# Kernel optimization log

Measured on AMD Instinct MI355X. Metric: run time of the kernel, lower is better.

The kernel has to match this reference:

```python
import jax, jax.numpy as jnp
import numpy as np

B, C, W, H, Z = 2, 32, 96, 96, 64
IC = C  # inter_channels defaults to in_channels (required by depthwise g conv)
THRESH = 1.5
EPS = 1e-5


def setup_inputs() -> dict:
    key = jax.random.key(0)
    ks = jax.random.split(key, 12)
    s1 = 1.0 / np.sqrt(C)   # 1x1x1 conv fan-in
    s3 = 1.0 / np.sqrt(3.0) # depthwise (1,1,3) conv fan-in per channel
    return {
        "x": jax.random.normal(ks[0], (B, C, W, H, Z), jnp.float32),
        # per-sample spacings in [0,3): mixes both branches around thresh 1.5
        "spacings": jax.random.uniform(ks[1], (B, 3), jnp.float32) * 3.0,
        "theta_w": jax.random.normal(ks[2], (IC, C), jnp.float32) * s1,
        "theta_b": jax.random.normal(ks[3], (IC,), jnp.float32) * s1,
        "phi_w": jax.random.normal(ks[4], (IC, C), jnp.float32) * s1,
        "phi_b": jax.random.normal(ks[5], (IC,), jnp.float32) * s1,
        "g_w": jax.random.normal(ks[6], (C, 3), jnp.float32) * s3,   # depthwise kernel along z
        "g_b": jax.random.normal(ks[7], (C,), jnp.float32) * s3,
        "W_w": jax.random.normal(ks[8], (C, IC), jnp.float32) * s1,
        "W_b": jax.random.normal(ks[9], (C,), jnp.float32) * s1,
        # torch inits BN gamma=0, beta=0 (zero-init residual trick); use small random
        "bn_gamma": jax.random.normal(ks[10], (C,), jnp.float32) * 0.1,
        "bn_beta": jax.random.normal(ks[11], (C,), jnp.float32) * 0.1,
    }


def _cvec(v):
    return v.reshape(1, -1, 1, 1, 1)


def _conv1x1(h, w, b):
    # 1x1x1 Conv3d == channel-mixing matmul
    return jnp.einsum('bcwhz,oc->bowhz', h, w) + _cvec(b)


def reference(x, spacings, theta_w, theta_b, phi_w, phi_b, g_w, g_b, W_w, W_b, bn_gamma, bn_beta):
    # theta/phi: 1x1x1 convs -> (B, IC, W, H, Z)
    t = _conv1x1(x, theta_w, theta_b)
    p = _conv1x1(x, phi_w, phi_b)

    # g: depthwise conv along z, kernel 3, pad 1 (groups=C)
    xp = jnp.pad(x, ((0, 0), (0, 0), (0, 0), (0, 0), (1, 1)))
    gx = (xp[..., :-2] * _cvec(g_w[:, 0])
          + xp[..., 1:-1] * _cvec(g_w[:, 1])
          + xp[..., 2:] * _cvec(g_w[:, 2])
          + _cvec(g_b))

    # non-local attention along z per (b, w, h) row: scores (B, W, H, Z, Z)
    f = jnp.einsum('bcwhz,bcwhy->bwhzy', t, p)
    a = jax.nn.softmax(f, axis=-1)
    y = jnp.einsum('bwhzy,bcwhy->bcwhz', a, gx)
    nl = y + x  # residual inside compute_x

    # per-sample branch on z-spacing, vectorized with where
    mask = (spacings[:, -1] <= THRESH).reshape(-1, 1, 1, 1, 1)
    res = jnp.where(mask, nl, x)

    # W: 1x1x1 conv + BatchNorm3d (training-mode batch stats)
    out = _conv1x1(res, W_w, W_b)
    mean = jnp.mean(out, axis=(0, 2, 3, 4), keepdims=True)
    var = jnp.var(out, axis=(0, 2, 3, 4), keepdims=True)
    out = (out - mean) * jax.lax.rsqrt(var + EPS)
    return out * _cvec(bn_gamma) + _cvec(bn_beta)
```

## Files before the change

kernel.cpp:

```cpp
#include <hip/hip_runtime.h>
#include <stdint.h>

#define CHS 589824
#define ROWS 18432
#define WHn 9216
#define NRED 1179648.0f
#define LOG2E 1.4426950408889634f

typedef short s16x8 __attribute__((ext_vector_type(8)));
typedef float f32x4v __attribute__((ext_vector_type(4)));

#define MFMA16 __builtin_amdgcn_mfma_f32_16x16x32_bf16

#define WSFRAG 10240

#define OXH 0
#define OP  8704
#define OG  13312
#define ROWL 17664
#define LDSZ (2*ROWL)

static __device__ __forceinline__ uint16_t bfh(float v) {
    union { __bf16 h; uint16_t u; } c; c.h = (__bf16)v; return c.u;
}
static __device__ __forceinline__ float bf2f(uint16_t u) {
    union { uint32_t x; float f; } c; c.x = (uint32_t)u << 16; return c.f;
}
static __device__ __forceinline__ uint32_t pk2u(uint16_t a, uint16_t b) {
    return (uint32_t)a | ((uint32_t)b << 16);
}
static __device__ __forceinline__ uint32_t pkbf(float a, float b) {
    return pk2u(bfh(a), bfh(b));
}
static __device__ __forceinline__ float ex2(float x) {
    float r;
    asm("v_exp_f32 %0, %1" : "=v"(r) : "v"(x));
    return r;
}
static __device__ __forceinline__ s16x8 rd8(const char* p) {
    union { uint64_t q[2]; s16x8 s; } v;
    v.q[0] = *(const uint64_t*)p;
    v.q[1] = *(const uint64_t*)(p + 8);
    return v.s;
}

static __device__ __forceinline__ void wfrag2(const float* __restrict__ Wp, int mt, int l15, int kb,
                                              float sc, s16x8& hi, s16x8& lo) {
    const float* p = Wp + (l15 + 16*mt)*32 + 8*kb;
    const float4 f0 = *(const float4*)p;
    const float4 f1 = *(const float4*)(p + 4);
    float f[8] = {f0.x*sc, f0.y*sc, f0.z*sc, f0.w*sc, f1.x*sc, f1.y*sc, f1.z*sc, f1.w*sc};
    union { uint32_t u[4]; s16x8 v; } rh, rl;
    #pragma unroll
    for (int i = 0; i < 4; ++i) {
        const uint16_t h0 = bfh(f[2*i]), h1 = bfh(f[2*i+1]);
        rh.u[i] = pk2u(h0, h1);
        rl.u[i] = pk2u(bfh(f[2*i] - bf2f(h0)), bfh(f[2*i+1] - bf2f(h1)));
    }
    hi = rh.v; lo = rl.v;
}
static __device__ __forceinline__ s16x8 wfragW(const float* __restrict__ Wp, int mt, int l15, int kb) {
    const float* p = Wp + (l15 + 16*mt)*32;
    const float4 f0 = *(const float4*)(p + 4*kb);
    const float4 f1 = *(const float4*)(p + 16 + 4*kb);
    union { uint32_t u[4]; s16x8 v; } r;
    r.u[0] = pkbf(f0.x, f0.y); r.u[1] = pkbf(f0.z, f0.w);
    r.u[2] = pkbf(f1.x, f1.y); r.u[3] = pkbf(f1.z, f1.w);
    return r.v;
}

__global__ __launch_bounds__(256) void k0_frag(
    const float* __restrict__ theta_w, const float* __restrict__ phi_w,
    const float* __restrict__ Ww, char* __restrict__ ws)
{
    const int tid = threadIdx.x;
    const int m = tid >> 7;
    const int r = tid & 127;
    const int mt = r >> 6, l = r & 63;
    s16x8 hi, lo;
    wfrag2(m ? phi_w : theta_w, mt, l & 15, l >> 4, m ? 1.0f : LOG2E, hi, lo);
    *(s16x8*)(ws + m*4096 + (mt*64 + l)*16)        = hi;
    *(s16x8*)(ws + m*4096 + 2048 + (mt*64 + l)*16) = lo;
    if (tid < 128) {
        const int mtw = tid >> 6, lw = tid & 63;
        *(s16x8*)(ws + 8192 + (mtw*64 + lw)*16) = wfragW(Ww, mtw, lw & 15, lw >> 4);
    }
}

__global__ __launch_bounds__(256, 4) void k1_row(
    const float* __restrict__ x, const float* __restrict__ spacings,
    const float* __restrict__ theta_b, const float* __restrict__ phi_b,
    const float* __restrict__ g_w, const float* __restrict__ g_b,
    const float* __restrict__ Wb, const char* __restrict__ frags,
    float* __restrict__ out, float* __restrict__ part)
{
    __shared__ __align__(16) char lds[LDSZ];
    const int t = threadIdx.x;
    const int wv = t >> 6, l = t & 63;
    const int l15 = l & 15, kb = l >> 4;
    const int row0 = blockIdx.x*2;
    const int b = row0 / WHn, wh = row0 - b*WHn;
    const long base = (long)b*32*CHS + (long)wh*64;
    const int zr = 16*wv + l15;

    #pragma unroll
    for (int rr = 0; rr < 2; ++rr) {
        char* L = lds + rr*ROWL;
        const float* xp = x + base + rr*64;
        float xv[8];
        #pragma unroll
        for (int j = 0; j < 8; ++j) xv[j] = xp[(long)(8*wv + j)*CHS + l];
        #pragma unroll
        for (int j = 0; j < 4; ++j) {
            const uint16_t h0 = bfh(xv[2*j]), h1 = bfh(xv[2*j+1]);
            *(uint32_t*)(L + OXH + l*136 + (8*wv + 2*j)*2)      = pk2u(h0, h1);
            *(uint32_t*)(L + OXH + l*136 + 64 + (8*wv + 2*j)*2) =
                pk2u(bfh(xv[2*j] - bf2f(h0)), bfh(xv[2*j+1] - bf2f(h1)));
        }
        const int pG = 32*(l >> 5) + 8*((l >> 2) & 3) + 4*((l >> 4) & 1) + (l & 3);
        #pragma unroll
        for (int j = 0; j < 8; ++j) {
            const int c = 8*wv + j;
            float xm = __shfl_up(xv[j], 1);   if (l == 0)  xm = 0.f;
            float xp2 = __shfl_down(xv[j], 1); if (l == 63) xp2 = 0.f;
            const float g = g_w[3*c]*xm + g_w[3*c+1]*xv[j] + g_w[3*c+2]*xp2 + g_b[c];
            *(uint16_t*)(L + OG + c*136 + 2*pG) = bfh(g);
        }
    }
    __syncthreads();

    s16x8 bth[2], btl[2];
    {
        s16x8 bxh[2], bxl[2];
        #pragma unroll
        for (int rr = 0; rr < 2; ++rr) {
            bxh[rr] = rd8(lds + rr*ROWL + OXH + zr*136 + 16*kb);
            bxl[rr] = rd8(lds + rr*ROWL + OXH + zr*136 + 64 + 16*kb);
        }
        {
            const s16x8 t0h = *(const s16x8*)(frags + l*16);
            const s16x8 t1h = *(const s16x8*)(frags + 1024 + l*16);
            const s16x8 t0l = *(const s16x8*)(frags + 2048 + l*16);
            const s16x8 t1l = *(const s16x8*)(frags + 3072 + l*16);
            const float4 b0 = *(const float4*)(theta_b + 4*kb);
            const float4 b1 = *(const float4*)(theta_b + 16 + 4*kb);
            #pragma unroll
            for (int rr = 0; rr < 2; ++rr) {
                f32x4v T0; T0[0]=b0.x*LOG2E; T0[1]=b0.y*LOG2E; T0[2]=b0.z*LOG2E; T0[3]=b0.w*LOG2E;
                f32x4v T1; T1[0]=b1.x*LOG2E; T1[1]=b1.y*LOG2E; T1[2]=b1.z*LOG2E; T1[3]=b1.w*LOG2E;
                T0 = MFMA16(t0h, bxh[rr], T0, 0, 0, 0);
                T0 = MFMA16(t0h, bxl[rr], T0, 0, 0, 0);
                T0 = MFMA16(t0l, bxh[rr], T0, 0, 0, 0);
                T1 = MFMA16(t1h, bxh[rr], T1, 0, 0, 0);
                T1 = MFMA16(t1h, bxl[rr], T1, 0, 0, 0);
                T1 = MFMA16(t1l, bxh[rr], T1, 0, 0, 0);
                uint16_t h[8];
                #pragma unroll
                for (int r = 0; r < 4; ++r) { h[r] = bfh(T0[r]); h[4+r] = bfh(T1[r]); }
                union { uint32_t u[4]; s16x8 s; } H, L2;
                H.u[0] = pk2u(h[0], h[1]); H.u[1] = pk2u(h[2], h[3]);
                H.u[2] = pk2u(h[4], h[5]); H.u[3] = pk2u(h[6], h[7]);
                L2.u[0] = pkbf(T0[0]-bf2f(h[0]), T0[1]-bf2f(h[1]));
                L2.u[1] = pkbf(T0[2]-bf2f(h[2]), T0[3]-bf2f(h[3]));
                L2.u[2] = pkbf(T1[0]-bf2f(h[4]), T1[1]-bf2f(h[5]));
                L2.u[3] = pkbf(T1[2]-bf2f(h[6]), T1[3]-bf2f(h[7]));
                bth[rr] = H.s; btl[rr] = L2.s;
            }
        }
        {
            const s16x8 p0h = *(const s16x8*)(frags + 4096 + l*16);
            const s16x8 p1h = *(const s16x8*)(frags + 4096 + 1024 + l*16);
            const s16x8 p0l = *(const s16x8*)(frags + 4096 + 2048 + l*16);
            const s16x8 p1l = *(const s16x8*)(frags + 4096 + 3072 + l*16);
            const float4 c0 = *(const float4*)(phi_b + 4*kb);
            const float4 c1 = *(const float4*)(phi_b + 16 + 4*kb);
            #pragma unroll
            for (int rr = 0; rr < 2; ++rr) {
                f32x4v P0; P0[0]=c0.x; P0[1]=c0.y; P0[2]=c0.z; P0[3]=c0.w;
                f32x4v P1; P1[0]=c1.x; P1[1]=c1.y; P1[2]=c1.z; P1[3]=c1.w;
                P0 = MFMA16(p0h, bxh[rr], P0, 0, 0, 0);
                P0 = MFMA16(p0h, bxl[rr], P0, 0, 0, 0);
                P0 = MFMA16(p0l, bxh[rr], P0, 0, 0, 0);
                P1 = MFMA16(p1h, bxh[rr], P1, 0, 0, 0);
                P1 = MFMA16(p1h, bxl[rr], P1, 0, 0, 0);
                P1 = MFMA16(p1l, bxh[rr], P1, 0, 0, 0);
                union { uint32_t u[2]; uint64_t q; } w;
                w.u[0] = pkbf(P0[0], P0[1]); w.u[1] = pkbf(P0[2], P0[3]);
                *(uint64_t*)(lds + rr*ROWL + OP + zr*72 + 16*kb) = w.q;
                w.u[0] = pkbf(P1[0], P1[1]); w.u[1] = pkbf(P1[2], P1[3]);
                *(uint64_t*)(lds + rr*ROWL + OP + zr*72 + 16*kb + 8) = w.q;
            }
        }
    }
    __syncthreads();

    f32x4v Fq[2][4];
    #pragma unroll
    for (int yt = 0; yt < 4; ++yt) {
        #pragma unroll
        for (int rr = 0; rr < 2; ++rr) {
            const s16x8 pah = rd8(lds + rr*ROWL + OP + (16*yt + l15)*72 + 16*kb);
            f32x4v zz; zz[0]=0.f; zz[1]=0.f; zz[2]=0.f; zz[3]=0.f;
            zz = MFMA16(pah, bth[rr], zz, 0, 0, 0);
            zz = MFMA16(pah, btl[rr], zz, 0, 0, 0);
            Fq[rr][yt] = zz;
        }
    }

    s16x8 apk[2][2];
    float inv[2];
    #pragma unroll
    for (int rr = 0; rr < 2; ++rr) {
        float mx = -3.4e38f;
        #pragma unroll
        for (int yt = 0; yt < 4; ++yt)
            #pragma unroll
            for (int r = 0; r < 4; ++r) mx = fmaxf(mx, Fq[rr][yt][r]);
        mx = fmaxf(mx, __shfl_xor(mx, 16));
        mx = fmaxf(mx, __shfl_xor(mx, 32));
        float p[4][4]; float sum = 0.f;
        #pragma unroll
        for (int yt = 0; yt < 4; ++yt)
            #pragma unroll
            for (int r = 0; r < 4; ++r) { p[yt][r] = ex2(Fq[rr][yt][r] - mx); sum += p[yt][r]; }
        sum += __shfl_xor(sum, 16);
        sum += __shfl_xor(sum, 32);
        inv[rr] = 1.0f / sum;
        #pragma unroll
        for (int ks = 0; ks < 2; ++ks) {
            union { uint32_t u[4]; s16x8 s; } A;
            A.u[0] = pkbf(p[2*ks][0],   p[2*ks][1]);
            A.u[1] = pkbf(p[2*ks][2],   p[2*ks][3]);
            A.u[2] = pkbf(p[2*ks+1][0], p[2*ks+1][1]);
            A.u[3] = pkbf(p[2*ks+1][2], p[2*ks+1][3]);
            apk[rr][ks] = A.s;
        }
    }

    const bool msk = spacings[b*3 + 2] <= 1.5f;
    s16x8 brf[2];
    #pragma unroll
    for (int rr = 0; rr < 2; ++rr) {
        f32x4v Yq[2];
        #pragma unroll
        for (int r = 0; r < 4; ++r) { Yq[0][r] = 0.f; Yq[1][r] = 0.f; }
        #pragma unroll
        for (int ks = 0; ks < 2; ++ks) {
            #pragma unroll
            for (int mt = 0; mt < 2; ++mt) {
                const s16x8 gA = rd8(lds + rr*ROWL + OG + (16*mt + l15)*136 + 64*ks + 16*kb);
                Yq[mt] = MFMA16(gA, apk[rr][ks], Yq[mt], 0, 0, 0);
            }
        }
        union { uint32_t u[4]; s16x8 s; } R;
        #pragma unroll
        for (int mt = 0; mt < 2; ++mt) {
            const uint64_t xh = *(const uint64_t*)(lds + rr*ROWL + OXH + zr*136 + (16*mt + 4*kb)*2);
            float rv[4];
            #pragma unroll
            for (int r = 0; r < 4; ++r) {
                const float xr = bf2f((uint16_t)(xh >> (16*r)));
                rv[r] = msk ? fmaf(Yq[mt][r], inv[rr], xr) : xr;
            }
            R.u[2*mt]   = pkbf(rv[0], rv[1]);
            R.u[2*mt+1] = pkbf(rv[2], rv[3]);
        }
        brf[rr] = R.s;
    }

    {
        const s16x8 aW0 = *(const s16x8*)(frags + 8192 + l*16);
        const s16x8 aW1 = *(const s16x8*)(frags + 8192 + (64 + l)*16);
        const float4 wb0 = *(const float4*)(Wb + 4*kb);
        const float4 wb1 = *(const float4*)(Wb + 16 + 4*kb);
        #pragma unroll
        for (int rr = 0; rr < 2; ++rr) {
            f32x4v accs[2];
            f32x4v a0; a0[0]=wb0.x; a0[1]=wb0.y; a0[2]=wb0.z; a0[3]=wb0.w;
            f32x4v a1; a1[0]=wb1.x; a1[1]=wb1.y; a1[2]=wb1.z; a1[3]=wb1.w;
            accs[0] = MFMA16(aW0, brf[rr], a0, 0, 0, 0);
            accs[1] = MFMA16(aW1, brf[rr], a1, 0, 0, 0);
            float* op = out + base + rr*64 + zr;
            #pragma unroll
            for (int mt = 0; mt < 2; ++mt)
                #pragma unroll
                for (int r = 0; r < 4; ++r)
                    op[(long)(16*mt + 4*kb + r)*CHS] = accs[mt][r];
            const int sr = (row0 + rr)*4 + wv;
            float bs[8];
            #pragma unroll
            for (int mt = 0; mt < 2; ++mt)
                #pragma unroll
                for (int r = 0; r < 4; ++r) bs[4*mt+r] = accs[mt][r];
            #pragma unroll
            for (int off = 1; off < 16; off <<= 1)
                #pragma unroll
                for (int i = 0; i < 8; ++i) bs[i] += __shfl_xor(bs[i], off);
            if (l15 == 0) {
                #pragma unroll
                for (int mt = 0; mt < 2; ++mt)
                    #pragma unroll
                    for (int r = 0; r < 4; ++r)
                        part[sr*64 + 16*mt + 4*kb + r] = bs[4*mt+r];
            }
            #pragma unroll
            for (int mt = 0; mt < 2; ++mt)
                #pragma unroll
                for (int r = 0; r < 4; ++r) { const float v = accs[mt][r]; bs[4*mt+r] = v*v; }
            #pragma unroll
            for (int off = 1; off < 16; off <<= 1)
                #pragma unroll
                for (int i = 0; i < 8; ++i) bs[i] += __shfl_xor(bs[i], off);
            if (l15 == 0) {
                #pragma unroll
                for (int mt = 0; mt < 2; ++mt)
                    #pragma unroll
                    for (int r = 0; r < 4; ++r)
                        part[sr*64 + 32 + 16*mt + 4*kb + r] = bs[4*mt+r];
            }
        }
    }
}

__global__ __launch_bounds__(256) void k2a(const float* __restrict__ part,
                                           float* __restrict__ part2)
{
    __shared__ float red[4][64];
    const int t = threadIdx.x, lane = t & 63, grp = t >> 6;
    const int p = blockIdx.x;
    float s = 0.f;
    for (int k = 0; k < 72; ++k) s += part[(p*288 + grp + 4*k)*64 + lane];
    red[grp][lane] = s;
    __syncthreads();
    if (t < 64) part2[p*64 + t] = red[0][t] + red[1][t] + red[2][t] + red[3][t];
}

__global__ __launch_bounds__(256) void k2b(const float* __restrict__ part2,
    const float* __restrict__ gamma, const float* __restrict__ beta,
    float* __restrict__ sc)
{
    __shared__ float red[4][64];
    __shared__ float tot[64];
    const int t = threadIdx.x, lane = t & 63, grp = t >> 6;
    float s = 0.f;
    for (int k = 0; k < 64; ++k) s += part2[(grp + 4*k)*64 + lane];
    red[grp][lane] = s;
    __syncthreads();
    if (t < 64) tot[t] = red[0][t] + red[1][t] + red[2][t] + red[3][t];
    __syncthreads();
    if (t < 32) {
        const float mean = tot[t] / NRED;
        const float var  = tot[32+t] / NRED - mean*mean;
        const float rstd = rsqrtf(var + 1e-5f);
        const float scale = gamma[t] * rstd;
        sc[t]    = scale;
        sc[32+t] = fmaf(-mean, scale, beta[t]);
    }
}

__global__ __launch_bounds__(256) void k3_norm(float* __restrict__ out,
                                               const float* __restrict__ sc)
{
    __shared__ float s[64];
    if (threadIdx.x < 64) s[threadIdx.x] = sc[threadIdx.x];
    __syncthreads();
    const int total4 = 2*32*CHS/4;
    const int Q = CHS/4;
    for (int i = blockIdx.x*256 + threadIdx.x; i < total4; i += gridDim.x*256) {
        float4 v = ((const float4*)out)[i];
        const int c = (i / Q) & 31;
        const float scale = s[c], shift = s[32+c];
        v.x = fmaf(v.x, scale, shift);
        v.y = fmaf(v.y, scale, shift);
        v.z = fmaf(v.z, scale, shift);
        v.w = fmaf(v.w, scale, shift);
        ((float4*)out)[i] = v;
    }
}

extern "C" void kernel_launch(void* const* d_in, const int* in_sizes, int n_in,
                              void* d_out, int out_size, void* d_ws, size_t ws_size,
                              hipStream_t stream) {
    const float* x        = (const float*)d_in[0];
    const float* spacings = (const float*)d_in[1];
    const float* theta_w  = (const float*)d_in[2];
    const float* theta_b  = (const float*)d_in[3];
    const float* phi_w    = (const float*)d_in[4];
    const float* phi_b    = (const float*)d_in[5];
    const float* g_w      = (const float*)d_in[6];
    const float* g_b      = (const float*)d_in[7];
    const float* Ww       = (const float*)d_in[8];
    const float* Wb       = (const float*)d_in[9];
    const float* gamma    = (const float*)d_in[10];
    const float* beta     = (const float*)d_in[11];
    float* out   = (float*)d_out;
    char*  frags = (char*)d_ws;
    float* part  = (float*)((char*)d_ws + WSFRAG);
    float* part2 = part + (size_t)ROWS*256;
    float* sc    = part2 + 256*64;

    hipLaunchKernelGGL(k0_frag, dim3(1), dim3(256), 0, stream, theta_w, phi_w, Ww, frags);
    hipLaunchKernelGGL(k1_row, dim3(ROWS/2), dim3(256), 0, stream,
                       x, spacings, theta_b, phi_b, g_w, g_b, Wb, frags, out, part);
    hipLaunchKernelGGL(k2a, dim3(256), dim3(256), 0, stream, part, part2);
    hipLaunchKernelGGL(k2b, dim3(1), dim3(256), 0, stream, part2, gamma, beta, sc);
    hipLaunchKernelGGL(k3_norm, dim3(4096), dim3(256), 0, stream, out, sc);
}
```

Baseline: 178.4 us.

## Load x directly into MFMA fragment registers and drop x staging in LDS

Each lane now loads x in the channel permutation the MFMA B-operand expects, builds the bf16 hi/lo fragments in registers, and reuses them for the residual. This removes the x region from LDS and one barrier. The halved LDS footprint lets the launch bound rise to 8 blocks per CU. The g-conv weights are pre-permuted in k0, and halo values at 16-lane boundaries are fetched with extra global loads, which adds uncoalesced-ish reads of x.

```diff
diff --git a/kernel.cpp b/kernel.cpp
--- a/kernel.cpp
+++ b/kernel.cpp
@@ -12,12 +12,11 @@
 
 #define MFMA16 __builtin_amdgcn_mfma_f32_16x16x32_bf16
 
-#define WSFRAG 10240
-
-#define OXH 0
-#define OP  8704
-#define OG  13312
-#define ROWL 17664
+#define WSFRAG 10752
+
+#define OP 0
+#define OG 4608
+#define ROWL 8960
 #define LDSZ (2*ROWL)
 
 static __device__ __forceinline__ uint16_t bfh(float v) {
@@ -46,9 +45,9 @@
 
 static __device__ __forceinline__ void wfrag2(const float* __restrict__ Wp, int mt, int l15, int kb,
                                               float sc, s16x8& hi, s16x8& lo) {
-    const float* p = Wp + (l15 + 16*mt)*32 + 8*kb;
-    const float4 f0 = *(const float4*)p;
-    const float4 f1 = *(const float4*)(p + 4);
+    const float* p = Wp + (l15 + 16*mt)*32;
+    const float4 f0 = *(const float4*)(p + 4*kb);
+    const float4 f1 = *(const float4*)(p + 16 + 4*kb);
     float f[8] = {f0.x*sc, f0.y*sc, f0.z*sc, f0.w*sc, f1.x*sc, f1.y*sc, f1.z*sc, f1.w*sc};
     union { uint32_t u[4]; s16x8 v; } rh, rl;
     #pragma unroll
@@ -71,7 +70,8 @@
 
 __global__ __launch_bounds__(256) void k0_frag(
     const float* __restrict__ theta_w, const float* __restrict__ phi_w,
-    const float* __restrict__ Ww, char* __restrict__ ws)
+    const float* __restrict__ Ww, const float* __restrict__ g_w,
+    const float* __restrict__ g_b, char* __restrict__ ws)
 {
     const int tid = threadIdx.x;
     const int m = tid >> 7;
@@ -85,12 +85,17 @@
         const int mtw = tid >> 6, lw = tid & 63;
         *(s16x8*)(ws + 8192 + (mtw*64 + lw)*16) = wfragW(Ww, mtw, lw & 15, lw >> 4);
     }
-}
-
-__global__ __launch_bounds__(256, 4) void k1_row(
+    if (tid < 32) {
+        const int kb = tid >> 3, i = tid & 7;
+        const int c = (i < 4) ? (4*kb + i) : (16 + 4*kb + i - 4);
+        float4 g = make_float4(g_w[3*c], g_w[3*c+1], g_w[3*c+2], g_b[c]);
+        *(float4*)(ws + 10240 + tid*16) = g;
+    }
+}
+
+__global__ __launch_bounds__(256, 8) void k1_row(
     const float* __restrict__ x, const float* __restrict__ spacings,
     const float* __restrict__ theta_b, const float* __restrict__ phi_b,
-    const float* __restrict__ g_w, const float* __restrict__ g_b,
     const float* __restrict__ Wb, const char* __restrict__ frags,
     float* __restrict__ out, float* __restrict__ part)
 {
@@ -102,127 +107,127 @@
     const int b = row0 / WHn, wh = row0 - b*WHn;
     const long base = (long)b*32*CHS + (long)wh*64;
     const int zr = 16*wv + l15;
-
+    const int pG = 32*(zr >> 5) + 8*((zr >> 2) & 3) + 4*((zr >> 4) & 1) + (zr & 3);
+
+    uint32_t xhw[2][4];
+    s16x8 bxl[2];
     #pragma unroll
     for (int rr = 0; rr < 2; ++rr) {
         char* L = lds + rr*ROWL;
         const float* xp = x + base + rr*64;
         float xv[8];
         #pragma unroll
-        for (int j = 0; j < 8; ++j) xv[j] = xp[(long)(8*wv + j)*CHS + l];
-        #pragma unroll
-        for (int j = 0; j < 4; ++j) {
-            const uint16_t h0 = bfh(xv[2*j]), h1 = bfh(xv[2*j+1]);
-            *(uint32_t*)(L + OXH + l*136 + (8*wv + 2*j)*2)      = pk2u(h0, h1);
-            *(uint32_t*)(L + OXH + l*136 + 64 + (8*wv + 2*j)*2) =
-                pk2u(bfh(xv[2*j] - bf2f(h0)), bfh(xv[2*j+1] - bf2f(h1)));
-        }
-        const int pG = 32*(l >> 5) + 8*((l >> 2) & 3) + 4*((l >> 4) & 1) + (l & 3);
-        #pragma unroll
-        for (int j = 0; j < 8; ++j) {
-            const int c = 8*wv + j;
-            float xm = __shfl_up(xv[j], 1);   if (l == 0)  xm = 0.f;
-            float xp2 = __shfl_down(xv[j], 1); if (l == 63) xp2 = 0.f;
-            const float g = g_w[3*c]*xm + g_w[3*c+1]*xv[j] + g_w[3*c+2]*xp2 + g_b[c];
+        for (int i = 0; i < 8; ++i) {
+            const int c = (i < 4) ? (4*kb + i) : (16 + 4*kb + i - 4);
+            xv[i] = xp[(long)c*CHS + zr];
+        }
+        #pragma unroll
+        for (int i = 0; i < 8; ++i) {
+            const int c = (i < 4) ? (4*kb + i) : (16 + 4*kb + i - 4);
+            const float4 gt = *(const float4*)(frags + 10240 + (kb*8 + i)*16);
+            float xm = __shfl_up(xv[i], 1);
+            float xq = __shfl_down(xv[i], 1);
+            if (l15 == 0)  xm = (zr > 0)  ? xp[(long)c*CHS + zr - 1] : 0.f;
+            if (l15 == 15) xq = (zr < 63) ? xp[(long)c*CHS + zr + 1] : 0.f;
+            const float g = fmaf(gt.x, xm, fmaf(gt.y, xv[i], fmaf(gt.z, xq, gt.w)));
             *(uint16_t*)(L + OG + c*136 + 2*pG) = bfh(g);
         }
-    }
-    __syncthreads();
+        union { uint32_t u[4]; s16x8 s; } H, LL;
+        #pragma unroll
+        for (int i2 = 0; i2 < 4; ++i2) {
+            const uint16_t h0 = bfh(xv[2*i2]), h1 = bfh(xv[2*i2+1]);
+            H.u[i2]  = pk2u(h0, h1);
+            LL.u[i2] = pk2u(bfh(xv[2*i2] - bf2f(h0)), bfh(xv[2*i2+1] - bf2f(h1)));
+        }
+        xhw[rr][0] = H.u[0]; xhw[rr][1] = H.u[1];
+        xhw[rr][2] = H.u[2]; xhw[rr][3] = H.u[3];
+        bxl[rr] = LL.s;
+    }
 
     s16x8 bth[2], btl[2];
     {
-        s16x8 bxh[2], bxl[2];
+        const s16x8 t0h = *(const s16x8*)(frags + l*16);
+        const s16x8 t1h = *(const s16x8*)(frags + 1024 + l*16);
+        const s16x8 t0l = *(const s16x8*)(frags + 2048 + l*16);
+        const s16x8 t1l = *(const s16x8*)(frags + 3072 + l*16);
+        const float4 b0 = *(const float4*)(theta_b + 4*kb);
+        const float4 b1 = *(const float4*)(theta_b + 16 + 4*kb);
         #pragma unroll
         for (int rr = 0; rr < 2; ++rr) {
-            bxh[rr] = rd8(lds + rr*ROWL + OXH + zr*136 + 16*kb);
-            bxl[rr] = rd8(lds + rr*ROWL + OXH + zr*136 + 64 + 16*kb);
-        }
-        {
-            const s16x8 t0h = *(const s16x8*)(frags + l*16);
-            const s16x8 t1h = *(const s16x8*)(frags + 1024 + l*16);
-            const s16x8 t0l = *(const s16x8*)(frags + 2048 + l*16);
-            const s16x8 t1l = *(const s16x8*)(frags + 3072 + l*16);
-            const float4 b0 = *(const float4*)(theta_b + 4*kb);
-            const float4 b1 = *(const float4*)(theta_b + 16 + 4*kb);
-            #pragma unroll
-            for (int rr = 0; rr < 2; ++rr) {
-                f32x4v T0; T0[0]=b0.x*LOG2E; T0[1]=b0.y*LOG2E; T0[2]=b0.z*LOG2E; T0[3]=b0.w*LOG2E;
-                f32x4v T1; T1[0]=b1.x*LOG2E; T1[1]=b1.y*LOG2E; T1[2]=b1.z*LOG2E; T1[3]=b1.w*LOG2E;
-                T0 = MFMA16(t0h, bxh[rr], T0, 0, 0, 0);
-                T0 = MFMA16(t0h, bxl[rr], T0, 0, 0, 0);
-                T0 = MFMA16(t0l, bxh[rr], T0, 0, 0, 0);
-                T1 = MFMA16(t1h, bxh[rr], T1, 0, 0, 0);
-                T1 = MFMA16(t1h, bxl[rr], T1, 0, 0, 0);
-                T1 = MFMA16(t1l, bxh[rr], T1, 0, 0, 0);
-                uint16_t h[8];
-                #pragma unroll
-                for (int r = 0; r < 4; ++r) { h[r] = bfh(T0[r]); h[4+r] = bfh(T1[r]); }
-                union { uint32_t u[4]; s16x8 s; } H, L2;
-                H.u[0] = pk2u(h[0], h[1]); H.u[1] = pk2u(h[2], h[3]);
-                H.u[2] = pk2u(h[4], h[5]); H.u[3] = pk2u(h[6], h[7]);
-                L2.u[0] = pkbf(T0[0]-bf2f(h[0]), T0[1]-bf2f(h[1]));
-                L2.u[1] = pkbf(T0[2]-bf2f(h[2]), T0[3]-bf2f(h[3]));
-                L2.u[2] = pkbf(T1[0]-bf2f(h[4]), T1[1]-bf2f(h[5]));
-                L2.u[3] = pkbf(T1[2]-bf2f(h[6]), T1[3]-bf2f(h[7]));
-                bth[rr] = H.s; btl[rr] = L2.s;
-            }
-        }
-        {
-            const s16x8 p0h = *(const s16x8*)(frags + 4096 + l*16);
-            const s16x8 p1h = *(const s16x8*)(frags + 4096 + 1024 + l*16);
-            const s16x8 p0l = *(const s16x8*)(frags + 4096 + 2048 + l*16);
-            const s16x8 p1l = *(const s16x8*)(frags + 4096 + 3072 + l*16);
-            const float4 c0 = *(const float4*)(phi_b + 4*kb);
-            const float4 c1 = *(const float4*)(phi_b + 16 + 4*kb);
-            #pragma unroll
-            for (int rr = 0; rr < 2; ++rr) {
-                f32x4v P0; P0[0]=c0.x; P0[1]=c0.y; P0[2]=c0.z; P0[3]=c0.w;
-                f32x4v P1; P1[0]=c1.x; P1[1]=c1.y; P1[2]=c1.z; P1[3]=c1.w;
-                P0 = MFMA16(p0h, bxh[rr], P0, 0, 0, 0);
-                P0 = MFMA16(p0h, bxl[rr], P0, 0, 0, 0);
-                P0 = MFMA16(p0l, bxh[rr], P0, 0, 0, 0);
-                P1 = MFMA16(p1h, bxh[rr], P1, 0, 0, 0);
-                P1 = MFMA16(p1h, bxl[rr], P1, 0, 0, 0);
-                P1 = MFMA16(p1l, bxh[rr], P1, 0, 0, 0);
-                union { uint32_t u[2]; uint64_t q; } w;
-                w.u[0] = pkbf(P0[0], P0[1]); w.u[1] = pkbf(P0[2], P0[3]);
-                *(uint64_t*)(lds + rr*ROWL + OP + zr*72 + 16*kb) = w.q;
-                w.u[0] = pkbf(P1[0], P1[1]); w.u[1] = pkbf(P1[2], P1[3]);
-                *(uint64_t*)(lds + rr*ROWL + OP + zr*72 + 16*kb + 8) = w.q;
-            }
+            union { uint32_t u[4]; s16x8 s; } BH;
+            BH.u[0]=xhw[rr][0]; BH.u[1]=xhw[rr][1]; BH.u[2]=xhw[rr][2]; BH.u[3]=xhw[rr][3];
+            f32x4v T0; T0[0]=b0.x*LOG2E; T0[1]=b0.y*LOG2E; T0[2]=b0.z*LOG2E; T0[3]=b0.w*LOG2E;
+            f32x4v T1; T1[0]=b1.x*LOG2E; T1[1]=b1.y*LOG2E; T1[2]=b1.z*LOG2E; T1[3]=b1.w*LOG2E;
+            T0 = MFMA16(t0h, BH.s, T0, 0, 0, 0);
+            T0 = MFMA16(t0h, bxl[rr], T0, 0, 0, 0);
+            T0 = MFMA16(t0l, BH.s, T0, 0, 0, 0);
+            T1 = MFMA16(t1h, BH.s, T1, 0, 0, 0);
+            T1 = MFMA16(t1h, bxl[rr], T1, 0, 0, 0);
+            T1 = MFMA16(t1l, BH.s, T1, 0, 0, 0);
+            uint16_t h[8];
+            #pragma unroll
+            for (int r = 0; r < 4; ++r) { h[r] = bfh(T0[r]); h[4+r] = bfh(T1[r]); }
+            union { uint32_t u[4]; s16x8 s; } H, L2;
+            H.u[0] = pk2u(h[0], h[1]); H.u[1] = pk2u(h[2], h[3]);
+            H.u[2] = pk2u(h[4], h[5]); H.u[3] = pk2u(h[6], h[7]);
+            L2.u[0] = pkbf(T0[0]-bf2f(h[0]), T0[1]-bf2f(h[1]));
+            L2.u[1] = pkbf(T0[2]-bf2f(h[2]), T0[3]-bf2f(h[3]));
+            L2.u[2] = pkbf(T1[0]-bf2f(h[4]), T1[1]-bf2f(h[5]));
+            L2.u[3] = pkbf(T1[2]-bf2f(h[6]), T1[3]-bf2f(h[7]));
+            bth[rr] = H.s; btl[rr] = L2.s;
+        }
+        const s16x8 p0h = *(const s16x8*)(frags + 4096 + l*16);
+        const s16x8 p1h = *(const s16x8*)(frags + 4096 + 1024 + l*16);
+        const s16x8 p0l = *(const s16x8*)(frags + 4096 + 2048 + l*16);
+        const s16x8 p1l = *(const s16x8*)(frags + 4096 + 3072 + l*16);
+        const float4 c0 = *(const float4*)(phi_b + 4*kb);
+        const float4 c1 = *(const float4*)(phi_b + 16 + 4*kb);
+        #pragma unroll
+        for (int rr = 0; rr < 2; ++rr) {
+            union { uint32_t u[4]; s16x8 s; } BH;
+            BH.u[0]=xhw[rr][0]; BH.u[1]=xhw[rr][1]; BH.u[2]=xhw[rr][2]; BH.u[3]=xhw[rr][3];
+            f32x4v P0; P0[0]=c0.x; P0[1]=c0.y; P0[2]=c0.z; P0[3]=c0.w;
+            f32x4v P1; P1[0]=c1.x; P1[1]=c1.y; P1[2]=c1.z; P1[3]=c1.w;
+            P0 = MFMA16(p0h, BH.s, P0, 0, 0, 0);
+            P0 = MFMA16(p0h, bxl[rr], P0, 0, 0, 0);
+            P0 = MFMA16(p0l, BH.s, P0, 0, 0, 0);
+            P1 = MFMA16(p1h, BH.s, P1, 0, 0, 0);
+            P1 = MFMA16(p1h, bxl[rr], P1, 0, 0, 0);
+            P1 = MFMA16(p1l, BH.s, P1, 0, 0, 0);
+            union { uint32_t u[2]; uint64_t q; } w;
+            w.u[0] = pkbf(P0[0], P0[1]); w.u[1] = pkbf(P0[2], P0[3]);
+            *(uint64_t*)(lds + rr*ROWL + OP + zr*72 + 16*kb) = w.q;
+            w.u[0] = pkbf(P1[0], P1[1]); w.u[1] = pkbf(P1[2], P1[3]);
+            *(uint64_t*)(lds + rr*ROWL + OP + zr*72 + 16*kb + 8) = w.q;
         }
     }
     __syncthreads();
 
-    f32x4v Fq[2][4];
+    s16x8 apk[2][2];
+    float inv[2];
     #pragma unroll
-    for (int yt = 0; yt < 4; ++yt) {
-        #pragma unroll
-        for (int rr = 0; rr < 2; ++rr) {
+    for (int rr = 0; rr < 2; ++rr) {
+        f32x4v Fq[4];
+        #pragma unroll
+        for (int yt = 0; yt < 4; ++yt) {
             const s16x8 pah = rd8(lds + rr*ROWL + OP + (16*yt + l15)*72 + 16*kb);
             f32x4v zz; zz[0]=0.f; zz[1]=0.f; zz[2]=0.f; zz[3]=0.f;
             zz = MFMA16(pah, bth[rr], zz, 0, 0, 0);
             zz = MFMA16(pah, btl[rr], zz, 0, 0, 0);
-            Fq[rr][yt] = zz;
-        }
-    }
-
-    s16x8 apk[2][2];
-    float inv[2];
-    #pragma unroll
-    for (int rr = 0; rr < 2; ++rr) {
+            Fq[yt] = zz;
+        }
         float mx = -3.4e38f;
         #pragma unroll
         for (int yt = 0; yt < 4; ++yt)
             #pragma unroll
-            for (int r = 0; r < 4; ++r) mx = fmaxf(mx, Fq[rr][yt][r]);
+            for (int r = 0; r < 4; ++r) mx = fmaxf(mx, Fq[yt][r]);
         mx = fmaxf(mx, __shfl_xor(mx, 16));
         mx = fmaxf(mx, __shfl_xor(mx, 32));
         float p[4][4]; float sum = 0.f;
         #pragma unroll
         for (int yt = 0; yt < 4; ++yt)
             #pragma unroll
-            for (int r = 0; r < 4; ++r) { p[yt][r] = ex2(Fq[rr][yt][r] - mx); sum += p[yt][r]; }
+            for (int r = 0; r < 4; ++r) { p[yt][r] = ex2(Fq[yt][r] - mx); sum += p[yt][r]; }
         sum += __shfl_xor(sum, 16);
         sum += __shfl_xor(sum, 32);
         inv[rr] = 1.0f / sum;
@@ -255,11 +260,11 @@
         union { uint32_t u[4]; s16x8 s; } R;
         #pragma unroll
         for (int mt = 0; mt < 2; ++mt) {
-            const uint64_t xh = *(const uint64_t*)(lds + rr*ROWL + OXH + zr*136 + (16*mt + 4*kb)*2);
             float rv[4];
             #pragma unroll
             for (int r = 0; r < 4; ++r) {
-                const float xr = bf2f((uint16_t)(xh >> (16*r)));
+                const uint32_t wd = xhw[rr][(4*mt + r) >> 1];
+                const float xr = bf2f((uint16_t)(wd >> (16*(r & 1))));
                 rv[r] = msk ? fmaf(Yq[mt][r], inv[rr], xr) : xr;
             }
             R.u[2*mt]   = pkbf(rv[0], rv[1]);
@@ -399,9 +404,10 @@
     float* part2 = part + (size_t)ROWS*256;
     float* sc    = part2 + 256*64;
 
-    hipLaunchKernelGGL(k0_frag, dim3(1), dim3(256), 0, stream, theta_w, phi_w, Ww, frags);
+    hipLaunchKernelGGL(k0_frag, dim3(1), dim3(256), 0, stream,
+                       theta_w, phi_w, Ww, g_w, g_b, frags);
     hipLaunchKernelGGL(k1_row, dim3(ROWS/2), dim3(256), 0, stream,
-                       x, spacings, theta_b, phi_b, g_w, g_b, Wb, frags, out, part);
+                       x, spacings, theta_b, phi_b, Wb, frags, out, part);
     hipLaunchKernelGGL(k2a, dim3(256), dim3(256), 0, stream, part, part2);
     hipLaunchKernelGGL(k2b, dim3(1), dim3(256), 0, stream, part2, gamma, beta, sc);
     hipLaunchKernelGGL(k3_norm, dim3(4096), dim3(256), 0, stream, out, sc);
```

New measurement: 295.4 us. +65.6%, slower.

## Alias g buffer onto x-low LDS region to shrink shared memory and raise occupancy

Applied to the files above, without the earlier changes.

Splits the x hi/lo bf16 planes into separate regions with a tighter row stride. The depthwise g values are kept in registers until the theta/phi projection is done, then written over the x-low region, which is no longer needed. This cuts the per-block LDS footprint so five blocks fit per CU instead of four, and the launch bound is raised to match. In exchange it adds an extra __syncthreads, holds more live registers across the projection phase, and changes the LDS bank patterns.

```diff
diff --git a/kernel.cpp b/kernel.cpp
--- a/kernel.cpp
+++ b/kernel.cpp
@@ -15,9 +15,10 @@
 #define WSFRAG 10240
 
 #define OXH 0
-#define OP  8704
-#define OG  13312
-#define ROWL 17664
+#define OXL 4608
+#define OP  9216
+#define OG  OXL
+#define ROWL 13824
 #define LDSZ (2*ROWL)
 
 static __device__ __forceinline__ uint16_t bfh(float v) {
@@ -87,7 +88,7 @@
     }
 }
 
-__global__ __launch_bounds__(256, 4) void k1_row(
+__global__ __launch_bounds__(256, 5) void k1_row(
     const float* __restrict__ x, const float* __restrict__ spacings,
     const float* __restrict__ theta_b, const float* __restrict__ phi_b,
     const float* __restrict__ g_w, const float* __restrict__ g_b,
@@ -103,6 +104,7 @@
     const long base = (long)b*32*CHS + (long)wh*64;
     const int zr = 16*wv + l15;
 
+    uint32_t gpk[2][4];
     #pragma unroll
     for (int rr = 0; rr < 2; ++rr) {
         char* L = lds + rr*ROWL;
@@ -113,18 +115,22 @@
         #pragma unroll
         for (int j = 0; j < 4; ++j) {
             const uint16_t h0 = bfh(xv[2*j]), h1 = bfh(xv[2*j+1]);
-            *(uint32_t*)(L + OXH + l*136 + (8*wv + 2*j)*2)      = pk2u(h0, h1);
-            *(uint32_t*)(L + OXH + l*136 + 64 + (8*wv + 2*j)*2) =
+            *(uint32_t*)(L + OXH + l*72 + (8*wv + 2*j)*2) = pk2u(h0, h1);
+            *(uint32_t*)(L + OXL + l*72 + (8*wv + 2*j)*2) =
                 pk2u(bfh(xv[2*j] - bf2f(h0)), bfh(xv[2*j+1] - bf2f(h1)));
         }
-        const int pG = 32*(l >> 5) + 8*((l >> 2) & 3) + 4*((l >> 4) & 1) + (l & 3);
-        #pragma unroll
-        for (int j = 0; j < 8; ++j) {
-            const int c = 8*wv + j;
-            float xm = __shfl_up(xv[j], 1);   if (l == 0)  xm = 0.f;
-            float xp2 = __shfl_down(xv[j], 1); if (l == 63) xp2 = 0.f;
-            const float g = g_w[3*c]*xm + g_w[3*c+1]*xv[j] + g_w[3*c+2]*xp2 + g_b[c];
-            *(uint16_t*)(L + OG + c*136 + 2*pG) = bfh(g);
+        #pragma unroll
+        for (int j = 0; j < 4; ++j) {
+            uint16_t gh[2];
+            #pragma unroll
+            for (int e = 0; e < 2; ++e) {
+                const int jj = 2*j + e;
+                const int c = 8*wv + jj;
+                float xm = __shfl_up(xv[jj], 1);   if (l == 0)  xm = 0.f;
+                float xq = __shfl_down(xv[jj], 1); if (l == 63) xq = 0.f;
+                gh[e] = bfh(g_w[3*c]*xm + g_w[3*c+1]*xv[jj] + g_w[3*c+2]*xq + g_b[c]);
+            }
+            gpk[rr][j] = pk2u(gh[0], gh[1]);
         }
     }
     __syncthreads();
@@ -134,8 +140,8 @@
         s16x8 bxh[2], bxl[2];
         #pragma unroll
         for (int rr = 0; rr < 2; ++rr) {
-            bxh[rr] = rd8(lds + rr*ROWL + OXH + zr*136 + 16*kb);
-            bxl[rr] = rd8(lds + rr*ROWL + OXH + zr*136 + 64 + 16*kb);
+            bxh[rr] = rd8(lds + rr*ROWL + OXH + zr*72 + 16*kb);
+            bxl[rr] = rd8(lds + rr*ROWL + OXL + zr*72 + 16*kb);
         }
         {
             const s16x8 t0h = *(const s16x8*)(frags + l*16);
@@ -194,6 +200,20 @@
     }
     __syncthreads();
 
+    {
+        const int pG = 32*(l >> 5) + 8*((l >> 2) & 3) + 4*((l >> 4) & 1) + (l & 3);
+        #pragma unroll
+        for (int rr = 0; rr < 2; ++rr) {
+            char* L = lds + rr*ROWL;
+            #pragma unroll
+            for (int j = 0; j < 8; ++j) {
+                const int c = 8*wv + j;
+                *(uint16_t*)(L + OG + c*136 + 2*pG) =
+                    (uint16_t)(gpk[rr][j >> 1] >> (16*(j & 1)));
+            }
+        }
+    }
+
     f32x4v Fq[2][4];
     #pragma unroll
     for (int yt = 0; yt < 4; ++yt) {
@@ -236,6 +256,7 @@
             apk[rr][ks] = A.s;
         }
     }
+    __syncthreads();
 
     const bool msk = spacings[b*3 + 2] <= 1.5f;
     s16x8 brf[2];
@@ -255,7 +276,7 @@
         union { uint32_t u[4]; s16x8 s; } R;
         #pragma unroll
         for (int mt = 0; mt < 2; ++mt) {
-            const uint64_t xh = *(const uint64_t*)(lds + rr*ROWL + OXH + zr*136 + (16*mt + 4*kb)*2);
+            const uint64_t xh = *(const uint64_t*)(lds + rr*ROWL + OXH + zr*72 + (16*mt + 4*kb)*2);
             float rv[4];
             #pragma unroll
             for (int r = 0; r < 4; ++r) {
```

Measured after the change: 204.8 us. 14.8% more time.

## Process one z-row per 128-thread block and raise MFMA wave priority

Applied to the files above, without the earlier changes.

The main row kernel now handles one (b,w,h) row per block with two waves, where it used to handle two rows per block with four waves. Each wave now owns 32 z positions (two 16-wide tiles) instead of 16 positions of one row, so shared P and G fragments are reused across both tiles and LDS per block halves. s_setprio is also raised around the MFMA sections so matrix work gets issue priority over other waves. The intent is more resident blocks and better overlap of loads with MFMA, at the cost of more registers per thread (16 x values loaded at once) and twice as many blocks.

```diff
diff --git a/kernel.cpp b/kernel.cpp
--- a/kernel.cpp
+++ b/kernel.cpp
@@ -17,8 +17,7 @@
 #define OXH 0
 #define OP  8704
 #define OG  13312
-#define ROWL 17664
-#define LDSZ (2*ROWL)
+#define LDSZ 17664
 
 static __device__ __forceinline__ uint16_t bfh(float v) {
     union { __bf16 h; uint16_t u; } c; c.h = (__bf16)v; return c.u;
@@ -87,7 +86,7 @@
     }
 }
 
-__global__ __launch_bounds__(256, 4) void k1_row(
+__global__ __launch_bounds__(128, 4) void k1_row(
     const float* __restrict__ x, const float* __restrict__ spacings,
     const float* __restrict__ theta_b, const float* __restrict__ phi_b,
     const float* __restrict__ g_w, const float* __restrict__ g_b,
@@ -98,33 +97,33 @@
     const int t = threadIdx.x;
     const int wv = t >> 6, l = t & 63;
     const int l15 = l & 15, kb = l >> 4;
-    const int row0 = blockIdx.x*2;
-    const int b = row0 / WHn, wh = row0 - b*WHn;
+    const int row = blockIdx.x;
+    const int b = row / WHn, wh = row - b*WHn;
     const long base = (long)b*32*CHS + (long)wh*64;
-    const int zr = 16*wv + l15;
-
-    #pragma unroll
-    for (int rr = 0; rr < 2; ++rr) {
-        char* L = lds + rr*ROWL;
-        const float* xp = x + base + rr*64;
-        float xv[8];
-        #pragma unroll
-        for (int j = 0; j < 8; ++j) xv[j] = xp[(long)(8*wv + j)*CHS + l];
-        #pragma unroll
-        for (int j = 0; j < 4; ++j) {
+
+    float xv[16];
+    {
+        const float* xp = x + base;
+        #pragma unroll
+        for (int j = 0; j < 16; ++j) xv[j] = xp[(long)(16*wv + j)*CHS + l];
+    }
+    {
+        #pragma unroll
+        for (int j = 0; j < 8; ++j) {
+            const int c0 = 16*wv + 2*j;
             const uint16_t h0 = bfh(xv[2*j]), h1 = bfh(xv[2*j+1]);
-            *(uint32_t*)(L + OXH + l*136 + (8*wv + 2*j)*2)      = pk2u(h0, h1);
-            *(uint32_t*)(L + OXH + l*136 + 64 + (8*wv + 2*j)*2) =
+            *(uint32_t*)(lds + OXH + l*136 + c0*2)      = pk2u(h0, h1);
+            *(uint32_t*)(lds + OXH + l*136 + 64 + c0*2) =
                 pk2u(bfh(xv[2*j] - bf2f(h0)), bfh(xv[2*j+1] - bf2f(h1)));
         }
         const int pG = 32*(l >> 5) + 8*((l >> 2) & 3) + 4*((l >> 4) & 1) + (l & 3);
         #pragma unroll
-        for (int j = 0; j < 8; ++j) {
-            const int c = 8*wv + j;
-            float xm = __shfl_up(xv[j], 1);   if (l == 0)  xm = 0.f;
+        for (int j = 0; j < 16; ++j) {
+            const int c = 16*wv + j;
+            float xm = __shfl_up(xv[j], 1);    if (l == 0)  xm = 0.f;
             float xp2 = __shfl_down(xv[j], 1); if (l == 63) xp2 = 0.f;
             const float g = g_w[3*c]*xm + g_w[3*c+1]*xv[j] + g_w[3*c+2]*xp2 + g_b[c];
-            *(uint16_t*)(L + OG + c*136 + 2*pG) = bfh(g);
+            *(uint16_t*)(lds + OG + c*136 + 2*pG) = bfh(g);
         }
     }
     __syncthreads();
@@ -133,9 +132,10 @@
     {
         s16x8 bxh[2], bxl[2];
         #pragma unroll
-        for (int rr = 0; rr < 2; ++rr) {
-            bxh[rr] = rd8(lds + rr*ROWL + OXH + zr*136 + 16*kb);
-            bxl[rr] = rd8(lds + rr*ROWL + OXH + zr*136 + 64 + 16*kb);
+        for (int nt = 0; nt < 2; ++nt) {
+            const int zr = 32*wv + 16*nt + l15;
+            bxh[nt] = rd8(lds + OXH + zr*136 + 16*kb);
+            bxl[nt] = rd8(lds + OXH + zr*136 + 64 + 16*kb);
         }
         {
             const s16x8 t0h = *(const s16x8*)(frags + l*16);
@@ -145,15 +145,15 @@
             const float4 b0 = *(const float4*)(theta_b + 4*kb);
             const float4 b1 = *(const float4*)(theta_b + 16 + 4*kb);
             #pragma unroll
-            for (int rr = 0; rr < 2; ++rr) {
+            for (int nt = 0; nt < 2; ++nt) {
                 f32x4v T0; T0[0]=b0.x*LOG2E; T0[1]=b0.y*LOG2E; T0[2]=b0.z*LOG2E; T0[3]=b0.w*LOG2E;
                 f32x4v T1; T1[0]=b1.x*LOG2E; T1[1]=b1.y*LOG2E; T1[2]=b1.z*LOG2E; T1[3]=b1.w*LOG2E;
-                T0 = MFMA16(t0h, bxh[rr], T0, 0, 0, 0);
-                T0 = MFMA16(t0h, bxl[rr], T0, 0, 0, 0);
-                T0 = MFMA16(t0l, bxh[rr], T0, 0, 0, 0);
-                T1 = MFMA16(t1h, bxh[rr], T1, 0, 0, 0);
-                T1 = MFMA16(t1h, bxl[rr], T1, 0, 0, 0);
-                T1 = MFMA16(t1l, bxh[rr], T1, 0, 0, 0);
+                T0 = MFMA16(t0h, bxh[nt], T0, 0, 0, 0);
+                T0 = MFMA16(t0h, bxl[nt], T0, 0, 0, 0);
+                T0 = MFMA16(t0l, bxh[nt], T0, 0, 0, 0);
+                T1 = MFMA16(t1h, bxh[nt], T1, 0, 0, 0);
+                T1 = MFMA16(t1h, bxl[nt], T1, 0, 0, 0);
+                T1 = MFMA16(t1l, bxh[nt], T1, 0, 0, 0);
                 uint16_t h[8];
                 #pragma unroll
                 for (int r = 0; r < 4; ++r) { h[r] = bfh(T0[r]); h[4+r] = bfh(T1[r]); }
@@ -164,7 +164,7 @@
                 L2.u[1] = pkbf(T0[2]-bf2f(h[2]), T0[3]-bf2f(h[3]));
                 L2.u[2] = pkbf(T1[0]-bf2f(h[4]), T1[1]-bf2f(h[5]));
                 L2.u[3] = pkbf(T1[2]-bf2f(h[6]), T1[3]-bf2f(h[7]));
-                bth[rr] = H.s; btl[rr] = L2.s;
+                bth[nt] = H.s; btl[nt] = L2.s;
             }
         }
         {
@@ -175,57 +175,60 @@
             const float4 c0 = *(const float4*)(phi_b + 4*kb);
             const float4 c1 = *(const float4*)(phi_b + 16 + 4*kb);
             #pragma unroll
-            for (int rr = 0; rr < 2; ++rr) {
+            for (int nt = 0; nt < 2; ++nt) {
+                const int zr = 32*wv + 16*nt + l15;
                 f32x4v P0; P0[0]=c0.x; P0[1]=c0.y; P0[2]=c0.z; P0[3]=c0.w;
                 f32x4v P1; P1[0]=c1.x; P1[1]=c1.y; P1[2]=c1.z; P1[3]=c1.w;
-                P0 = MFMA16(p0h, bxh[rr], P0, 0, 0, 0);
-                P0 = MFMA16(p0h, bxl[rr], P0, 0, 0, 0);
-                P0 = MFMA16(p0l, bxh[rr], P0, 0, 0, 0);
-                P1 = MFMA16(p1h, bxh[rr], P1, 0, 0, 0);
-                P1 = MFMA16(p1h, bxl[rr], P1, 0, 0, 0);
-                P1 = MFMA16(p1l, bxh[rr], P1, 0, 0, 0);
+                P0 = MFMA16(p0h, bxh[nt], P0, 0, 0, 0);
+                P0 = MFMA16(p0h, bxl[nt], P0, 0, 0, 0);
+                P0 = MFMA16(p0l, bxh[nt], P0, 0, 0, 0);
+                P1 = MFMA16(p1h, bxh[nt], P1, 0, 0, 0);
+                P1 = MFMA16(p1h, bxl[nt], P1, 0, 0, 0);
+                P1 = MFMA16(p1l, bxh[nt], P1, 0, 0, 0);
                 union { uint32_t u[2]; uint64_t q; } w;
                 w.u[0] = pkbf(P0[0], P0[1]); w.u[1] = pkbf(P0[2], P0[3]);
-                *(uint64_t*)(lds + rr*ROWL + OP + zr*72 + 16*kb) = w.q;
+                *(uint64_t*)(lds + OP + zr*72 + 16*kb) = w.q;
                 w.u[0] = pkbf(P1[0], P1[1]); w.u[1] = pkbf(P1[2], P1[3]);
-                *(uint64_t*)(lds + rr*ROWL + OP + zr*72 + 16*kb + 8) = w.q;
+                *(uint64_t*)(lds + OP + zr*72 + 16*kb + 8) = w.q;
             }
         }
     }
     __syncthreads();
 
     f32x4v Fq[2][4];
+    __builtin_amdgcn_s_setprio(1);
     #pragma unroll
     for (int yt = 0; yt < 4; ++yt) {
-        #pragma unroll
-        for (int rr = 0; rr < 2; ++rr) {
-            const s16x8 pah = rd8(lds + rr*ROWL + OP + (16*yt + l15)*72 + 16*kb);
+        const s16x8 pah = rd8(lds + OP + (16*yt + l15)*72 + 16*kb);
+        #pragma unroll
+        for (int nt = 0; nt < 2; ++nt) {
             f32x4v zz; zz[0]=0.f; zz[1]=0.f; zz[2]=0.f; zz[3]=0.f;
-            zz = MFMA16(pah, bth[rr], zz, 0, 0, 0);
-            zz = MFMA16(pah, btl[rr], zz, 0, 0, 0);
-            Fq[rr][yt] = zz;
-        }
-    }
+            zz = MFMA16(pah, bth[nt], zz, 0, 0, 0);
+            zz = MFMA16(pah, btl[nt], zz, 0, 0, 0);
+            Fq[nt][yt] = zz;
+        }
+    }
+    __builtin_amdgcn_s_setprio(0);
 
     s16x8 apk[2][2];
     float inv[2];
     #pragma unroll
-    for (int rr = 0; rr < 2; ++rr) {
+    for (int nt = 0; nt < 2; ++nt) {
         float mx = -3.4e38f;
         #pragma unroll
         for (int yt = 0; yt < 4; ++yt)
             #pragma unroll
-            for (int r = 0; r < 4; ++r) mx = fmaxf(mx, Fq[rr][yt][r]);
+            for (int r = 0; r < 4; ++r) mx = fmaxf(mx, Fq[nt][yt][r]);
         mx = fmaxf(mx, __shfl_xor(mx, 16));
         mx = fmaxf(mx, __shfl_xor(mx, 32));
         float p[4][4]; float sum = 0.f;
         #pragma unroll
         for (int yt = 0; yt < 4; ++yt)
             #pragma unroll
-            for (int r = 0; r < 4; ++r) { p[yt][r] = ex2(Fq[rr][yt][r] - mx); sum += p[yt][r]; }
+            for (int r = 0; r < 4; ++r) { p[yt][r] = ex2(Fq[nt][yt][r] - mx); sum += p[yt][r]; }
         sum += __shfl_xor(sum, 16);
         sum += __shfl_xor(sum, 32);
-        inv[rr] = 1.0f / sum;
+        inv[nt] = 1.0f / sum;
         #pragma unroll
         for (int ks = 0; ks < 2; ++ks) {
             union { uint32_t u[4]; s16x8 s; } A;
@@ -233,39 +236,42 @@
             A.u[1] = pkbf(p[2*ks][2],   p[2*ks][3]);
             A.u[2] = pkbf(p[2*ks+1][0], p[2*ks+1][1]);
             A.u[3] = pkbf(p[2*ks+1][2], p[2*ks+1][3]);
-            apk[rr][ks] = A.s;
+            apk[nt][ks] = A.s;
         }
     }
 
     const bool msk = spacings[b*3 + 2] <= 1.5f;
     s16x8 brf[2];
     #pragma unroll
-    for (int rr = 0; rr < 2; ++rr) {
+    for (int nt = 0; nt < 2; ++nt) {
+        const int zr = 32*wv + 16*nt + l15;
         f32x4v Yq[2];
         #pragma unroll
         for (int r = 0; r < 4; ++r) { Yq[0][r] = 0.f; Yq[1][r] = 0.f; }
+        __builtin_amdgcn_s_setprio(1);
         #pragma unroll
         for (int ks = 0; ks < 2; ++ks) {
             #pragma unroll
             for (int mt = 0; mt < 2; ++mt) {
-                const s16x8 gA = rd8(lds + rr*ROWL + OG + (16*mt + l15)*136 + 64*ks + 16*kb);
-                Yq[mt] = MFMA16(gA, apk[rr][ks], Yq[mt], 0, 0, 0);
-            }
-        }
+                const s16x8 gA = rd8(lds + OG + (16*mt + l15)*136 + 64*ks + 16*kb);
+                Yq[mt] = MFMA16(gA, apk[nt][ks], Yq[mt], 0, 0, 0);
+            }
+        }
+        __builtin_amdgcn_s_setprio(0);
         union { uint32_t u[4]; s16x8 s; } R;
         #pragma unroll
         for (int mt = 0; mt < 2; ++mt) {
-            const uint64_t xh = *(const uint64_t*)(lds + rr*ROWL + OXH + zr*136 + (16*mt + 4*kb)*2);
+            const uint64_t xh = *(const uint64_t*)(lds + OXH + zr*136 + (16*mt + 4*kb)*2);
             float rv[4];
             #pragma unroll
             for (int r = 0; r < 4; ++r) {
                 const float xr = bf2f((uint16_t)(xh >> (16*r)));
-                rv[r] = msk ? fmaf(Yq[mt][r], inv[rr], xr) : xr;
+                rv[r] = msk ? fmaf(Yq[mt][r], inv[nt], xr) : xr;
             }
             R.u[2*mt]   = pkbf(rv[0], rv[1]);
             R.u[2*mt+1] = pkbf(rv[2], rv[3]);
         }
-        brf[rr] = R.s;
+        brf[nt] = R.s;
     }
 
     {
@@ -274,19 +280,22 @@
         const float4 wb0 = *(const float4*)(Wb + 4*kb);
         const float4 wb1 = *(const float4*)(Wb + 16 + 4*kb);
         #pragma unroll
-        for (int rr = 0; rr < 2; ++rr) {
+        for (int nt = 0; nt < 2; ++nt) {
+            const int zr = 32*wv + 16*nt + l15;
             f32x4v accs[2];
             f32x4v a0; a0[0]=wb0.x; a0[1]=wb0.y; a0[2]=wb0.z; a0[3]=wb0.w;
             f32x4v a1; a1[0]=wb1.x; a1[1]=wb1.y; a1[2]=wb1.z; a1[3]=wb1.w;
-            accs[0] = MFMA16(aW0, brf[rr], a0, 0, 0, 0);
-            accs[1] = MFMA16(aW1, brf[rr], a1, 0, 0, 0);
-            float* op = out + base + rr*64 + zr;
+            __builtin_amdgcn_s_setprio(1);
+            accs[0] = MFMA16(aW0, brf[nt], a0, 0, 0, 0);
+            accs[1] = MFMA16(aW1, brf[nt], a1, 0, 0, 0);
+            __builtin_amdgcn_s_setprio(0);
+            float* op = out + base + zr;
             #pragma unroll
             for (int mt = 0; mt < 2; ++mt)
                 #pragma unroll
                 for (int r = 0; r < 4; ++r)
                     op[(long)(16*mt + 4*kb + r)*CHS] = accs[mt][r];
-            const int sr = (row0 + rr)*4 + wv;
+            const int sr = row*4 + 2*wv + nt;
             float bs[8];
             #pragma unroll
             for (int mt = 0; mt < 2; ++mt)
@@ -400,7 +409,7 @@
     float* sc    = part2 + 256*64;
 
     hipLaunchKernelGGL(k0_frag, dim3(1), dim3(256), 0, stream, theta_w, phi_w, Ww, frags);
-    hipLaunchKernelGGL(k1_row, dim3(ROWS/2), dim3(256), 0, stream,
+    hipLaunchKernelGGL(k1_row, dim3(ROWS), dim3(128), 0, stream,
                        x, spacings, theta_b, phi_b, g_w, g_b, Wb, frags, out, part);
     hipLaunchKernelGGL(k2a, dim3(256), dim3(256), 0, stream, part, part2);
     hipLaunchKernelGGL(k2b, dim3(1), dim3(256), 0, stream, part2, gamma, beta, sc);
```

After: 171.8 us, median of 2. 1.04x faster.
